# Optimization experiments

Measured on AMD Instinct MI355X. Metric: run time of the kernel, lower is better.

The kernel has to match this reference:

```python
import jax, jax.numpy as jnp
import numpy as np

GROUPS = 2048   # number of FPS centroids S
K = 24          # ball-query neighbors
RADIUS = 0.2    # ball radius (xyz in unit cube)


def setup_inputs() -> dict:
    key = jax.random.key(0)
    k1, k2 = jax.random.split(key)
    xyz = jax.random.uniform(k1, (8, 8192, 3), dtype=jnp.float32)
    points = jax.random.normal(k2, (8, 8192, 128), dtype=jnp.float32)
    return {"xyz": xyz, "points": points}


def _fps(xyz, npoint):
    # iterative farthest point sampling; deterministic start at index 0
    B, N, _ = xyz.shape

    def step(carry, _):
        distance, farthest = carry                       # [B,N], [B]
        centroid = jnp.take_along_axis(xyz, farthest[:, None, None], axis=1)  # [B,1,3]
        d = jnp.sum((xyz - centroid) ** 2, axis=-1)      # [B,N]
        distance = jnp.minimum(distance, d)
        nxt = jnp.argmax(distance, axis=-1).astype(jnp.int32)
        return (distance, nxt), farthest

    init = (jnp.full((B, N), 1e10, jnp.float32), jnp.zeros((B,), jnp.int32))
    _, idxs = jax.lax.scan(step, init, None, length=npoint)  # [npoint,B]
    return jnp.transpose(idxs)                               # [B,npoint]


def _index_points(points, idx):
    # points [B,N,C], idx [B,...] -> [B,...,C]
    B = idx.shape[0]
    flat = idx.reshape(B, -1)
    out = jnp.take_along_axis(points, flat[..., None], axis=1)
    return out.reshape(*idx.shape, points.shape[-1])


def _square_distance(src, dst):
    # src [B,N,C], dst [B,M,C] -> [B,N,M]
    return (jnp.sum(src ** 2, -1)[..., None]
            + jnp.sum(dst ** 2, -1)[:, None, :]
            - 2.0 * jnp.einsum('bnc,bmc->bnm', src, dst))


def _query_ball(radius, nsample, xyz, new_xyz):
    B, N, _ = xyz.shape
    sqr = _square_distance(new_xyz, xyz)                 # [B,S,N]
    base = jnp.arange(N, dtype=jnp.int32)
    idx = jnp.where(sqr > radius * radius, jnp.int32(N), base)  # out-of-ball -> N
    idx = jnp.sort(idx, axis=-1)[..., :nsample]          # [B,S,k]
    first = idx[..., :1]
    return jnp.where(idx == N, first, idx)


def reference(xyz, points):
    B, N, _ = xyz.shape
    fps_idx = _fps(xyz, GROUPS)                          # [B,S]
    new_xyz = _index_points(xyz, fps_idx)                # [B,S,3]
    anchor_feat = _index_points(points, fps_idx)         # [B,S,D]
    idx = _query_ball(RADIUS, K, xyz, new_xyz)           # [B,S,k]
    grouped_xyz = _index_points(xyz, idx)                # [B,S,k,3]
    grouped_points = _index_points(points, idx)          # [B,S,k,D]
    grouped = jnp.concatenate([grouped_points, grouped_xyz], axis=-1)  # use_xyz=True
    anchor = jnp.broadcast_to(anchor_feat[:, :, None, :],
                              (B, GROUPS, K, points.shape[-1]))
    new_points = jnp.concatenate([grouped, anchor], axis=-1)  # [B,S,k,2D+3]
    return new_xyz, new_points
```

## Files before the change

kernel.cpp:

```cpp
#include <hip/hip_runtime.h>
#include <stdint.h>


#define NBATCH 8
#define NPTS   8192
#define NCH    128
#define NGROUP 2048
#define NK     24
#define ROWLEN (2 * NCH + 3)

#define FPS_T  512
#define PPT    16

typedef float v2f __attribute__((ext_vector_type(2)));

__device__ __forceinline__ float sq3_nofma(float dx, float dy, float dz) {
#pragma clang fp contract(off)
  return dx * dx + dy * dy + dz * dz;
}

__device__ __forceinline__ float dot3_fma(float ax, float ay, float az,
                                          float bx, float by, float bz) {
  float acc = __fmul_rn(ax, bx);
  acc = __fmaf_rn(ay, by, acc);
  acc = __fmaf_rn(az, bz, acc);
  return acc;
}

__device__ __forceinline__ float ballquery_sqr(float srcSq, float dstSq, float dot) {
#pragma clang fp contract(off)
  return (srcSq + dstSq) - 2.0f * dot;
}

template <int CTRL>
__device__ __forceinline__ float maxdpp(float v) {
  int s = __builtin_amdgcn_update_dpp(__builtin_bit_cast(int, v),
                                      __builtin_bit_cast(int, v),
                                      CTRL, 0xF, 0xF, false);
  return fmaxf(v, __builtin_bit_cast(float, s));
}

__device__ __forceinline__ float readlane_f(float v, int lane) {
  return __builtin_bit_cast(float,
      __builtin_amdgcn_readlane(__builtin_bit_cast(int, v), lane));
}

__global__ __launch_bounds__(FPS_T) void fps_kernel(const float* __restrict__ xyz,
                                                    int* __restrict__ fps_idx) {
  const int b = blockIdx.x;
  const int t = threadIdx.x;
  const int lane = t & 63;
  const int w = t >> 6;
  const float* xb = xyz + (size_t)b * NPTS * 3;

  __shared__ float s_xyz[NPTS * 3];
  __shared__ float s_v[2][8];
  __shared__ int   s_i[2][8];

  {
    const float4* src4 = (const float4*)xb;
    float4* dst4 = (float4*)s_xyz;
    for (int i = t; i < (NPTS * 3) / 4; i += FPS_T) dst4[i] = src4[i];
  }

  const int base = t * PPT;
  v2f px[8], py[8], pz[8], d2[8];
#pragma unroll
  for (int j = 0; j < 8; ++j) {
    const int n0 = base + 2 * j;
    px[j].x = xb[n0 * 3 + 0]; py[j].x = xb[n0 * 3 + 1]; pz[j].x = xb[n0 * 3 + 2];
    px[j].y = xb[n0 * 3 + 3]; py[j].y = xb[n0 * 3 + 4]; pz[j].y = xb[n0 * 3 + 5];
    d2[j].x = 1e10f; d2[j].y = 1e10f;
  }

  float cx = xb[0], cy = xb[1], cz = xb[2];
  if (t == 0) fps_idx[b * NGROUP + 0] = 0;

  for (int s = 1; s < NGROUP; ++s) {
    const int p = s & 1;

    float lv = -1.0f;
#pragma unroll
    for (int j = 0; j < 8; ++j) {
      v2f dx, dy, dz, dd, nd;
      {
#pragma clang fp contract(off)
        dx = px[j] - cx;
        dy = py[j] - cy;
        dz = pz[j] - cz;
        dd = dx * dx + dy * dy + dz * dz;
      }
      nd.x = fminf(d2[j].x, dd.x);
      nd.y = fminf(d2[j].y, dd.y);
      d2[j] = nd;
      lv = fmaxf(fmaxf(nd.x, nd.y), lv);
    }
    int kk = 0;
#pragma unroll
    for (int j = 7; j >= 0; --j) {
      if (d2[j].y == lv) kk = 2 * j + 1;
      if (d2[j].x == lv) kk = 2 * j;
    }
    const int li = base + kk;

    float v = lv;
    v = maxdpp<0x111>(v);
    v = maxdpp<0x112>(v);
    v = maxdpp<0x114>(v);
    v = maxdpp<0x118>(v);
    v = maxdpp<0x142>(v);
    v = maxdpp<0x143>(v);
    const float wmax = readlane_f(v, 63);
    const unsigned long long m = __ballot(lv == wmax);
    const int wl = (int)__builtin_ctzll(m);
    const int wli = __builtin_amdgcn_readlane(li, wl);
    if (lane == 0) { s_v[p][w] = wmax; s_i[p][w] = wli; }
    __syncthreads();

    float pv = (lane < 8) ? s_v[p][lane] : -1.0f;
    int   pi = (lane < 8) ? s_i[p][lane] : 0;
    float r = pv;
    r = maxdpp<0x111>(r);
    r = maxdpp<0x112>(r);
    r = maxdpp<0x114>(r);
    const float bmax = readlane_f(r, 7);
    const unsigned long long m2 = __ballot(pv == bmax);
    const int wwin = (int)__builtin_ctzll(m2);
    const int bi = __builtin_amdgcn_readlane(pi, wwin);

    if (t == 0) fps_idx[b * NGROUP + s] = bi;

    const int b3 = bi * 3;
    cx = s_xyz[b3 + 0];
    cy = s_xyz[b3 + 1];
    cz = s_xyz[b3 + 2];
  }
}

__global__ __launch_bounds__(256) void group_kernel(const float* __restrict__ xyz,
                                                    const float* __restrict__ points,
                                                    const int* __restrict__ fps_idx,
                                                    float* __restrict__ out) {
  const int gb = blockIdx.x;
  const int b = gb >> 11;
  const int tid = threadIdx.x;
  const float* xb = xyz + (size_t)b * NPTS * 3;
  const float* pb = points + (size_t)b * NPTS * NCH;

  __shared__ int s_idx[NK];

  const int a_idx = fps_idx[gb];
  const float cx = xb[a_idx * 3 + 0];
  const float cy = xb[a_idx * 3 + 1];
  const float cz = xb[a_idx * 3 + 2];
  const float srcSq = sq3_nofma(cx, cy, cz);
  const float R2 = (float)(0.2 * 0.2);

  if (tid < 64) {
    int cnt = 0;
    int first = 0;
    const unsigned long long below = ((unsigned long long)1 << tid) - 1ull;
    for (int chunk = 0; chunk < NPTS / 128; ++chunk) {
      const int n0 = (chunk << 7) + (tid << 1);
      const float* p = xb + (size_t)n0 * 3;
      const float2 A = *(const float2*)(p + 0);
      const float2 Bv = *(const float2*)(p + 2);
      const float2 C = *(const float2*)(p + 4);
      const float x0 = A.x, y0 = A.y, z0 = Bv.x;
      const float x1 = Bv.y, y1 = C.x, z1 = C.y;

      const float sqr0 = ballquery_sqr(srcSq, sq3_nofma(x0, y0, z0),
                                       dot3_fma(cx, cy, cz, x0, y0, z0));
      const float sqr1 = ballquery_sqr(srcSq, sq3_nofma(x1, y1, z1),
                                       dot3_fma(cx, cy, cz, x1, y1, z1));
      const bool ok0 = !(sqr0 > R2);
      const bool ok1 = !(sqr1 > R2);
      const unsigned long long m0 = __ballot(ok0);
      const unsigned long long m1 = __ballot(ok1);
      if (cnt == 0 && (m0 | m1)) {
        const int f0 = m0 ? (int)__builtin_ctzll(m0) : 64;
        const int f1 = m1 ? (int)__builtin_ctzll(m1) : 64;
        first = (f0 <= f1) ? ((chunk << 7) + 2 * f0) : ((chunk << 7) + 2 * f1 + 1);
      }
      const int p0 = cnt + (int)__popcll(m0 & below) + (int)__popcll(m1 & below);
      const int p1 = p0 + (ok0 ? 1 : 0);
      if (ok0 && p0 < NK) s_idx[p0] = n0;
      if (ok1 && p1 < NK) s_idx[p1] = n0 + 1;
      cnt += (int)__popcll(m0) + (int)__popcll(m1);
      if (cnt >= NK) break;
    }
    if (tid >= cnt && tid < NK) s_idx[tid] = first;
  }
  __syncthreads();

  if (tid == 0) {
    float* onx = out + (size_t)gb * 3;
    onx[0] = cx; onx[1] = cy; onx[2] = cz;
  }

  float* op = out + (size_t)NBATCH * NGROUP * 3 + (size_t)gb * (NK * ROWLEN);
  const float* anchor = pb + (size_t)a_idx * NCH;
  for (int e = tid; e < NK * ROWLEN; e += 256) {
    const int k = e / ROWLEN;
    const int c = e - k * ROWLEN;
    const int si = s_idx[k];
    float v;
    if (c < NCH)            v = pb[(size_t)si * NCH + c];
    else if (c < NCH + 3)   v = xb[si * 3 + (c - NCH)];
    else                    v = anchor[c - (NCH + 3)];
    op[e] = v;
  }
}

extern "C" void kernel_launch(void* const* d_in, const int* in_sizes, int n_in,
                              void* d_out, int out_size, void* d_ws, size_t ws_size,
                              hipStream_t stream) {
  const float* xyz = (const float*)d_in[0];
  const float* points = (const float*)d_in[1];
  float* out = (float*)d_out;
  int* fps_idx = (int*)d_ws;

  fps_kernel<<<dim3(NBATCH), dim3(FPS_T), 0, stream>>>(xyz, fps_idx);
  group_kernel<<<dim3(NBATCH * NGROUP), dim3(256), 0, stream>>>(xyz, points, fps_idx, out);
}
```

Before: 2.232 ms.

## Replace FPS cross-wave reduction with packed 64-bit LDS atomicMax key

```diff
diff --git a/kernel.cpp b/kernel.cpp
--- a/kernel.cpp
+++ b/kernel.cpp
@@ -50,18 +50,17 @@
   const int b = blockIdx.x;
   const int t = threadIdx.x;
   const int lane = t & 63;
-  const int w = t >> 6;
   const float* xb = xyz + (size_t)b * NPTS * 3;
 
   __shared__ float s_xyz[NPTS * 3];
-  __shared__ float s_v[2][8];
-  __shared__ int   s_i[2][8];
+  __shared__ unsigned long long s_key[2];
 
   {
     const float4* src4 = (const float4*)xb;
     float4* dst4 = (float4*)s_xyz;
     for (int i = t; i < (NPTS * 3) / 4; i += FPS_T) dst4[i] = src4[i];
   }
+  if (t == 0) { s_key[0] = 0ull; s_key[1] = 0ull; }
 
   const int base = t * PPT;
   v2f px[8], py[8], pz[8], d2[8];
@@ -76,9 +75,9 @@
   float cx = xb[0], cy = xb[1], cz = xb[2];
   if (t == 0) fps_idx[b * NGROUP + 0] = 0;
 
+  __syncthreads();
+
   for (int s = 1; s < NGROUP; ++s) {
-    const int p = s & 1;
-
     float lv = -1.0f;
 #pragma unroll
     for (int j = 0; j < 8; ++j) {
@@ -113,20 +112,18 @@
     const float wmax = readlane_f(v, 63);
     const unsigned long long m = __ballot(lv == wmax);
     const int wl = (int)__builtin_ctzll(m);
-    const int wli = __builtin_amdgcn_readlane(li, wl);
-    if (lane == 0) { s_v[p][w] = wmax; s_i[p][w] = wli; }
+
+    if (lane == wl) {
+      const unsigned long long key =
+          ((unsigned long long)(unsigned)s << 45) |
+          ((unsigned long long)__builtin_bit_cast(unsigned, lv) << 13) |
+          (unsigned long long)(unsigned)(8191 - li);
+      atomicMax(&s_key[s & 1], key);
+    }
     __syncthreads();
 
-    float pv = (lane < 8) ? s_v[p][lane] : -1.0f;
-    int   pi = (lane < 8) ? s_i[p][lane] : 0;
-    float r = pv;
-    r = maxdpp<0x111>(r);
-    r = maxdpp<0x112>(r);
-    r = maxdpp<0x114>(r);
-    const float bmax = readlane_f(r, 7);
-    const unsigned long long m2 = __ballot(pv == bmax);
-    const int wwin = (int)__builtin_ctzll(m2);
-    const int bi = __builtin_amdgcn_readlane(pi, wwin);
+    const unsigned long long gk = s_key[s & 1];
+    const int bi = 8191 - (int)(gk & 0x1fffu);
 
     if (t == 0) fps_idx[b * NGROUP + s] = bi;
 
@@ -141,7 +138,8 @@
                                                     const float* __restrict__ points,
                                                     const int* __restrict__ fps_idx,
                                                     float* __restrict__ out) {
-  const int gb = blockIdx.x;
+  const int bx = blockIdx.x;
+  const int gb = ((bx & 7) << 11) | (bx >> 3);
   const int b = gb >> 11;
   const int tid = threadIdx.x;
   const float* xb = xyz + (size_t)b * NPTS * 3;
```

Measured after the change: 2.620 ms. 17.4% more time.
